# Performance work log

Hardware: AMD Instinct MI355X
Metric: run time of the kernel (lower is better)

## Reference

```python
import jax, jax.numpy as jnp
import numpy as np

N_NODES = 20000
N_REL = 200
DIM = 128
N_EDGES = 200000
N_TIMES = 8


def setup_inputs() -> dict:
    key = jax.random.key(0)
    ks = jax.random.split(key, 12)
    s = 1.0 / np.sqrt(DIM)
    return {
        "edge_index": jax.random.randint(ks[0], (2, N_EDGES), 0, N_NODES),
        "edge_type": jax.random.randint(ks[1], (N_EDGES,), 0, N_REL),
        "edge_time": jax.random.randint(ks[2], (N_EDGES,), 0, N_TIMES),
        "edge_weight": jax.random.uniform(ks[3], (N_EDGES,), dtype=jnp.float32),
        "node_emb": jax.random.normal(ks[4], (N_NODES, DIM), dtype=jnp.float32),
        "rel_emb": jax.random.normal(ks[5], (N_REL, DIM), dtype=jnp.float32),
        "W_enc": jax.random.normal(ks[6], (DIM, DIM), dtype=jnp.float32) * s,
        "Wz": jax.random.normal(ks[7], (DIM, DIM), dtype=jnp.float32) * s,
        "Uz": jax.random.normal(ks[8], (DIM, DIM), dtype=jnp.float32) * s,
        "Wh": jax.random.normal(ks[9], (DIM, DIM), dtype=jnp.float32) * s,
        "Uh": jax.random.normal(ks[10], (DIM, DIM), dtype=jnp.float32) * s,
        "bz": jnp.zeros((DIM,), dtype=jnp.float32),
        "bh": jnp.zeros((DIM,), dtype=jnp.float32),
        "num_times": N_TIMES,
    }


def reference(edge_index, edge_type, edge_time, edge_weight,
              node_emb, rel_emb, W_enc, Wz, Uz, Wh, Uh, bz, bh, num_times):
    # TemporalEncoder.forward: loop over sorted unique timestamps; per-step
    # masked-edge GNN encode (R-GCN lite) then gated SSM cell; state detached.
    src, dst = edge_index[0], edge_index[1]
    rel_e = rel_emb[edge_type]          # [E, D] gather (constant across steps)
    src_e = node_emb[src]               # [E, D]
    n_nodes = node_emb.shape[0]

    def step(state, t):
        m = (edge_time == t).astype(edge_weight.dtype)       # [E]
        msg = src_e * rel_e * (edge_weight * m)[:, None]     # [E, D]
        agg = jax.ops.segment_sum(msg, dst, num_segments=n_nodes)  # [N, D]
        h = jnp.tanh(agg @ W_enc)                            # base_encoder output
        z = jax.nn.sigmoid(h @ Wz + state @ Uz + bz)
        cand = jnp.tanh(h @ Wh + state @ Uh + bh)
        new_state = (1.0 - z) * state + z * cand             # ssm.cell
        return jax.lax.stop_gradient(new_state), new_state   # state.detach()

    state0 = jnp.zeros_like(node_emb)
    _, outs = jax.lax.scan(step, state0, jnp.arange(num_times))
    return outs[-1]  # last_out, shape [N, D]
```

## Files before the change

kernel.cpp:

```cpp
#include <hip/hip_runtime.h>

#define N_NODES 20000
#define N_EDGES 200000
#define DIM 128
#define T_STEPS 8
#define N_TILES (N_NODES / 16)
#define SCAN_N (N_NODES + 1)
#define SCAN_BLKS ((SCAN_N + 1023) / 1024)

typedef short short8 __attribute__((ext_vector_type(8)));
typedef float f32x4 __attribute__((ext_vector_type(4)));

static __device__ __forceinline__ unsigned short f2bf(float f) {
  union { float f; unsigned u; } v; v.f = f;
  unsigned r = v.u + 0x7fffu + ((v.u >> 16) & 1u);
  return (unsigned short)(r >> 16);
}
static __device__ __forceinline__ float fast_tanh(float x) {
  float e = __expf(2.f * x);
  return 1.f - 2.f / (e + 1.f);
}
static __device__ __forceinline__ float fast_sig(float x) {
  return 1.f / (1.f + __expf(-x));
}

__global__ void repack5(const float* __restrict__ w0,
                        const float* __restrict__ w1,
                        const float* __restrict__ w2,
                        const float* __restrict__ w3,
                        const float* __restrict__ w4,
                        unsigned short* __restrict__ pack) {
  int i = blockIdx.x * blockDim.x + threadIdx.x;
  if (i >= 5 * 16384) return;
  int m = i >> 14, r = i & 16383;
  int j = r & 7, lane = (r >> 3) & 63, ks = (r >> 9) & 3, nt = (r >> 11) & 7;
  int n = nt * 16 + (lane & 15);
  int k = ks * 32 + (lane >> 4) * 8 + j;
  const float* w = (m == 0) ? w0 : (m == 1) ? w1 : (m == 2) ? w2
                 : (m == 3) ? w3 : w4;
  pack[i] = f2bf(w[k * DIM + n]);
}

__global__ void hist_k(const int* __restrict__ dst, int* __restrict__ counts) {
  int i = blockIdx.x * blockDim.x + threadIdx.x;
  if (i >= N_EDGES) return;
  atomicAdd(&counts[dst[i]], 1);
}

__global__ void scan1_k(const int* __restrict__ counts,
                        int* __restrict__ base, int* __restrict__ bsum) {
  __shared__ int ls[256];
  int tid = threadIdx.x;
  int i0 = blockIdx.x * 1024 + tid * 4;
  int v[4], ts = 0;
#pragma unroll
  for (int r = 0; r < 4; r++) {
    v[r] = (i0 + r < SCAN_N) ? counts[i0 + r] : 0;
    ts += v[r];
  }
  ls[tid] = ts; __syncthreads();
#pragma unroll
  for (int off = 1; off < 256; off <<= 1) {
    int x = (tid >= off) ? ls[tid - off] : 0;
    __syncthreads(); ls[tid] += x; __syncthreads();
  }
  int run = ls[tid] - ts;
  if (tid == 255) bsum[blockIdx.x] = ls[255];
#pragma unroll
  for (int r = 0; r < 4; r++) {
    if (i0 + r < SCAN_N) base[i0 + r] = run;
    run += v[r];
  }
}

__global__ void scan2_k(int* __restrict__ bsum) {
  __shared__ int ls[256];
  int tid = threadIdx.x;
  int v = (tid < SCAN_BLKS) ? bsum[tid] : 0;
  ls[tid] = v; __syncthreads();
#pragma unroll
  for (int off = 1; off < 256; off <<= 1) {
    int x = (tid >= off) ? ls[tid - off] : 0;
    __syncthreads(); ls[tid] += x; __syncthreads();
  }
  if (tid < SCAN_BLKS) bsum[tid] = ls[tid] - v;
}

__global__ void scan3_k(int* __restrict__ base, const int* __restrict__ bsum) {
  int i = blockIdx.x * blockDim.x + threadIdx.x;
  if (i < SCAN_N) base[i] += bsum[i >> 10];
}

__global__ void fill_k(const int* __restrict__ src, const int* __restrict__ dst,
                       const int* __restrict__ etype, const int* __restrict__ etime,
                       const float* __restrict__ ew,
                       const int* __restrict__ base, int* __restrict__ cursor,
                       unsigned* __restrict__ epack, float* __restrict__ sw) {
  int i = blockIdx.x * blockDim.x + threadIdx.x;
  if (i >= N_EDGES) return;
  int d = dst[i];
  int pos = base[d] + atomicAdd(&cursor[d], 1);
  epack[pos] = (unsigned)src[i] | ((unsigned)etype[i] << 15) | ((unsigned)etime[i] << 23);
  sw[pos] = ew[i];
}

__global__ void gather_k(const int* __restrict__ base,
                         const unsigned* __restrict__ epack,
                         const float* __restrict__ sw,
                         const float* __restrict__ nemb,
                         const float* __restrict__ remb,
                         unsigned short* __restrict__ aggb) {
  int lane = threadIdx.x & 63;
  int node = (blockIdx.x * blockDim.x + threadIdx.x) >> 6;
  int s0 = base[node], s1 = base[node + 1];
  float ax[T_STEPS], ay[T_STEPS];
#pragma unroll
  for (int tt = 0; tt < T_STEPS; tt++) { ax[tt] = 0.f; ay[tt] = 0.f; }
  for (int i = s0; i < s1; i++) {
    unsigned u = epack[i];
    float w = sw[i];
    int s = u & 0x7fff, rt = (u >> 15) & 0xff, t = u >> 23;
    float2 sv = ((const float2*)(nemb + (size_t)s * DIM))[lane];
    float2 rv = ((const float2*)(remb + (size_t)rt * DIM))[lane];
    float m0 = sv.x * rv.x * w;
    float m1 = sv.y * rv.y * w;
#pragma unroll
    for (int tt = 0; tt < T_STEPS; tt++) {
      ax[tt] += (t == tt) ? m0 : 0.f;
      ay[tt] += (t == tt) ? m1 : 0.f;
    }
  }
#pragma unroll
  for (int tt = 0; tt < T_STEPS; tt++) {
    ushort2 o; o.x = f2bf(ax[tt]); o.y = f2bf(ay[tt]);
    ((ushort2*)(aggb + ((size_t)tt * N_NODES + node) * DIM))[lane] = o;
  }
}

__launch_bounds__(512)
__global__ void fused_recur(const unsigned short* __restrict__ aggb,
                            const unsigned short* __restrict__ pack,
                            const float* __restrict__ bz,
                            const float* __restrict__ bh,
                            float* __restrict__ out) {
  __shared__ unsigned short Hb[2][16 * 136];
  __shared__ unsigned short Sb[2][16 * 136];
  int lane = threadIdx.x & 63;
  int nt = threadIdx.x >> 6;
  int tile = blockIdx.x;
  int q = lane >> 4, l15 = lane & 15;
  int row0 = tile * 16;

  short8 wenc[4], wz[4], uz[4], wh[4], uh[4];
#pragma unroll
  for (int ks = 0; ks < 4; ks++) {
    int fo = ((nt * 4 + ks) * 64 + lane) * 8;
    wenc[ks] = *(const short8*)(pack + 16384 * 0 + fo);
    wz[ks]   = *(const short8*)(pack + 16384 * 1 + fo);
    uz[ks]   = *(const short8*)(pack + 16384 * 2 + fo);
    wh[ks]   = *(const short8*)(pack + 16384 * 3 + fo);
    uh[ks]   = *(const short8*)(pack + 16384 * 4 + fo);
  }
  float bzv = bz[nt * 16 + l15];
  float bhv = bh[nt * 16 + l15];

  f32x4 stC = (f32x4){0.f, 0.f, 0.f, 0.f};

  for (int t = 0; t < T_STEPS; t++) {
    f32x4 acch = (f32x4){0.f, 0.f, 0.f, 0.f};
#pragma unroll
    for (int ks = 0; ks < 4; ks++) {
      short8 aA = *(const short8*)(aggb +
          ((size_t)t * N_NODES + row0 + l15) * DIM + ks * 32 + q * 8);
      acch = __builtin_amdgcn_mfma_f32_16x16x32_bf16(aA, wenc[ks], acch, 0, 0, 0);
    }
    unsigned short* hB = Hb[t & 1];
    unsigned short* sB = Sb[t & 1];
#pragma unroll
    for (int r = 0; r < 4; r++) {
      hB[(q * 4 + r) * 136 + nt * 16 + l15] = f2bf(fast_tanh(acch[r]));
      sB[(q * 4 + r) * 136 + nt * 16 + l15] = f2bf(stC[r]);
    }
    __syncthreads();

    short8 hA[4], sA[4];
#pragma unroll
    for (int ks = 0; ks < 4; ks++) {
      hA[ks] = *(const short8*)&hB[l15 * 136 + ks * 32 + q * 8];
      sA[ks] = *(const short8*)&sB[l15 * 136 + ks * 32 + q * 8];
    }

    f32x4 accz = (f32x4){bzv, bzv, bzv, bzv};
    f32x4 accc = (f32x4){bhv, bhv, bhv, bhv};
#pragma unroll
    for (int ks = 0; ks < 4; ks++) {
      accz = __builtin_amdgcn_mfma_f32_16x16x32_bf16(hA[ks], wz[ks], accz, 0, 0, 0);
      accz = __builtin_amdgcn_mfma_f32_16x16x32_bf16(sA[ks], uz[ks], accz, 0, 0, 0);
      accc = __builtin_amdgcn_mfma_f32_16x16x32_bf16(hA[ks], wh[ks], accc, 0, 0, 0);
      accc = __builtin_amdgcn_mfma_f32_16x16x32_bf16(sA[ks], uh[ks], accc, 0, 0, 0);
    }
#pragma unroll
    for (int r = 0; r < 4; r++) {
      float z = fast_sig(accz[r]);
      float c = fast_tanh(accc[r]);
      stC[r] = (1.f - z) * stC[r] + z * c;
    }
  }

#pragma unroll
  for (int r = 0; r < 4; r++)
    out[(size_t)(row0 + q * 4 + r) * DIM + nt * 16 + l15] = stC[r];
}

extern "C" void kernel_launch(void* const* d_in, const int* in_sizes, int n_in,
                              void* d_out, int out_size, void* d_ws, size_t ws_size,
                              hipStream_t stream) {
  const int* eidx  = (const int*)d_in[0];
  const int* src   = eidx;
  const int* dst   = eidx + N_EDGES;
  const int* etype = (const int*)d_in[1];
  const int* etime = (const int*)d_in[2];
  const float* ew   = (const float*)d_in[3];
  const float* nemb = (const float*)d_in[4];
  const float* remb = (const float*)d_in[5];
  const float* Wenc = (const float*)d_in[6];
  const float* Wz   = (const float*)d_in[7];
  const float* Uz   = (const float*)d_in[8];
  const float* Wh   = (const float*)d_in[9];
  const float* Uh   = (const float*)d_in[10];
  const float* bz   = (const float*)d_in[11];
  const float* bh   = (const float*)d_in[12];

  unsigned short* aggb = (unsigned short*)d_ws;
  int* counts = (int*)(aggb + (size_t)T_STEPS * N_NODES * DIM);
  int* cursor = counts + SCAN_N;
  int* bsum   = cursor + N_NODES;
  int* base   = bsum + 64;
  unsigned* epack = (unsigned*)(base + SCAN_N);
  float* sw   = (float*)(epack + N_EDGES);
  unsigned short* pack = (unsigned short*)(sw + N_EDGES);
  float* outp = (float*)d_out;

  hipMemsetAsync(counts, 0, (size_t)(SCAN_N + N_NODES) * sizeof(int), stream);
  repack5<<<(5 * 16384 + 255) / 256, 256, 0, stream>>>(Wenc, Wz, Uz, Wh, Uh, pack);
  hist_k<<<(N_EDGES + 255) / 256, 256, 0, stream>>>(dst, counts);
  scan1_k<<<SCAN_BLKS, 256, 0, stream>>>(counts, base, bsum);
  scan2_k<<<1, 256, 0, stream>>>(bsum);
  scan3_k<<<(SCAN_N + 255) / 256, 256, 0, stream>>>(base, bsum);
  fill_k<<<(N_EDGES + 255) / 256, 256, 0, stream>>>(src, dst, etype, etime, ew,
                                                    base, cursor, epack, sw);
  gather_k<<<N_NODES / 4, 256, 0, stream>>>(base, epack, sw, nemb, remb, aggb);
  fused_recur<<<N_TILES, 512, 0, stream>>>(aggb, pack, bz, bh, outp);
}
```

Before: 223.1 us.

## Split encoder GEMM out of recurrence into separate fully parallel kernel

```diff
diff --git a/kernel.cpp b/kernel.cpp
--- a/kernel.cpp
+++ b/kernel.cpp
@@ -7,6 +7,7 @@
 #define N_TILES (N_NODES / 16)
 #define SCAN_N (N_NODES + 1)
 #define SCAN_BLKS ((SCAN_N + 1023) / 1024)
+#define LSTR 140
 
 typedef short short8 __attribute__((ext_vector_type(8)));
 typedef float f32x4 __attribute__((ext_vector_type(4)));
@@ -137,29 +138,64 @@
   }
 }
 
-__launch_bounds__(512)
-__global__ void fused_recur(const unsigned short* __restrict__ aggb,
-                            const unsigned short* __restrict__ pack,
-                            const float* __restrict__ bz,
-                            const float* __restrict__ bh,
-                            float* __restrict__ out) {
-  __shared__ unsigned short Hb[2][16 * 136];
-  __shared__ unsigned short Sb[2][16 * 136];
+__global__ void enc_H(const unsigned short* __restrict__ aggb,
+                      const unsigned short* __restrict__ pack,
+                      unsigned short* __restrict__ Hbuf) {
+  __shared__ unsigned short hl[4][16 * LSTR];
+  int lane = threadIdx.x & 63;
+  int w = blockIdx.x * 4 + (threadIdx.x >> 6);
+  int t = w & 7, tile = w >> 3;
+  int q = lane >> 4, l15 = lane & 15;
+  int row0 = tile * 16;
+
+  f32x4 acc[8];
+#pragma unroll
+  for (int nt = 0; nt < 8; nt++) acc[nt] = (f32x4){0.f, 0.f, 0.f, 0.f};
+#pragma unroll
+  for (int ks = 0; ks < 4; ks++) {
+    short8 a = *(const short8*)(aggb +
+        ((size_t)t * N_NODES + row0 + l15) * DIM + ks * 32 + q * 8);
+#pragma unroll
+    for (int nt = 0; nt < 8; nt++) {
+      short8 b = *(const short8*)(pack + ((nt * 4 + ks) * 64 + lane) * 8);
+      acc[nt] = __builtin_amdgcn_mfma_f32_16x16x32_bf16(a, b, acc[nt], 0, 0, 0);
+    }
+  }
+  unsigned short* h = hl[threadIdx.x >> 6];
+#pragma unroll
+  for (int nt = 0; nt < 8; nt++)
+#pragma unroll
+    for (int r = 0; r < 4; r++)
+      h[(q * 4 + r) * LSTR + nt * 16 + l15] = f2bf(fast_tanh(acc[nt][r]));
+  __syncthreads();
+#pragma unroll
+  for (int ks = 0; ks < 4; ks++) {
+    short8 v = *(const short8*)&h[l15 * LSTR + ks * 32 + q * 8];
+    *(short8*)(Hbuf + (((size_t)(tile * T_STEPS + t) * 4 + ks) * 64 + lane) * 8) = v;
+  }
+}
+
+__launch_bounds__(512, 4)
+__global__ void recur(const unsigned short* __restrict__ Hbuf,
+                      const unsigned short* __restrict__ pack,
+                      const float* __restrict__ bz,
+                      const float* __restrict__ bh,
+                      float* __restrict__ out) {
+  __shared__ unsigned short Sb[2][16 * LSTR];
   int lane = threadIdx.x & 63;
   int nt = threadIdx.x >> 6;
   int tile = blockIdx.x;
   int q = lane >> 4, l15 = lane & 15;
   int row0 = tile * 16;
 
-  short8 wenc[4], wz[4], uz[4], wh[4], uh[4];
+  short8 wz[4], uz[4], wh[4], uh[4];
 #pragma unroll
   for (int ks = 0; ks < 4; ks++) {
     int fo = ((nt * 4 + ks) * 64 + lane) * 8;
-    wenc[ks] = *(const short8*)(pack + 16384 * 0 + fo);
-    wz[ks]   = *(const short8*)(pack + 16384 * 1 + fo);
-    uz[ks]   = *(const short8*)(pack + 16384 * 2 + fo);
-    wh[ks]   = *(const short8*)(pack + 16384 * 3 + fo);
-    uh[ks]   = *(const short8*)(pack + 16384 * 4 + fo);
+    wz[ks] = *(const short8*)(pack + 16384 * 1 + fo);
+    uz[ks] = *(const short8*)(pack + 16384 * 2 + fo);
+    wh[ks] = *(const short8*)(pack + 16384 * 3 + fo);
+    uh[ks] = *(const short8*)(pack + 16384 * 4 + fo);
   }
   float bzv = bz[nt * 16 + l15];
   float bhv = bh[nt * 16 + l15];
@@ -167,28 +203,23 @@
   f32x4 stC = (f32x4){0.f, 0.f, 0.f, 0.f};
 
   for (int t = 0; t < T_STEPS; t++) {
-    f32x4 acch = (f32x4){0.f, 0.f, 0.f, 0.f};
-#pragma unroll
-    for (int ks = 0; ks < 4; ks++) {
-      short8 aA = *(const short8*)(aggb +
-          ((size_t)t * N_NODES + row0 + l15) * DIM + ks * 32 + q * 8);
-      acch = __builtin_amdgcn_mfma_f32_16x16x32_bf16(aA, wenc[ks], acch, 0, 0, 0);
-    }
-    unsigned short* hB = Hb[t & 1];
     unsigned short* sB = Sb[t & 1];
 #pragma unroll
-    for (int r = 0; r < 4; r++) {
-      hB[(q * 4 + r) * 136 + nt * 16 + l15] = f2bf(fast_tanh(acch[r]));
-      sB[(q * 4 + r) * 136 + nt * 16 + l15] = f2bf(stC[r]);
-    }
+    for (int r = 0; r < 4; r++)
+      sB[(q * 4 + r) * LSTR + nt * 16 + l15] = f2bf(stC[r]);
+
+    short8 hA[4];
+#pragma unroll
+    for (int ks = 0; ks < 4; ks++)
+      hA[ks] = *(const short8*)(Hbuf +
+          (((size_t)(tile * T_STEPS + t) * 4 + ks) * 64 + lane) * 8);
+
     __syncthreads();
 
-    short8 hA[4], sA[4];
-#pragma unroll
-    for (int ks = 0; ks < 4; ks++) {
-      hA[ks] = *(const short8*)&hB[l15 * 136 + ks * 32 + q * 8];
-      sA[ks] = *(const short8*)&sB[l15 * 136 + ks * 32 + q * 8];
-    }
+    short8 sA[4];
+#pragma unroll
+    for (int ks = 0; ks < 4; ks++)
+      sA[ks] = *(const short8*)&sB[l15 * LSTR + ks * 32 + q * 8];
 
     f32x4 accz = (f32x4){bzv, bzv, bzv, bzv};
     f32x4 accc = (f32x4){bhv, bhv, bhv, bhv};
@@ -232,7 +263,8 @@
   const float* bh   = (const float*)d_in[12];
 
   unsigned short* aggb = (unsigned short*)d_ws;
-  int* counts = (int*)(aggb + (size_t)T_STEPS * N_NODES * DIM);
+  unsigned short* Hbuf = aggb + (size_t)T_STEPS * N_NODES * DIM;
+  int* counts = (int*)(Hbuf + (size_t)T_STEPS * N_NODES * DIM);
   int* cursor = counts + SCAN_N;
   int* bsum   = cursor + N_NODES;
   int* base   = bsum + 64;
@@ -250,5 +282,6 @@
   fill_k<<<(N_EDGES + 255) / 256, 256, 0, stream>>>(src, dst, etype, etime, ew,
                                                     base, cursor, epack, sw);
   gather_k<<<N_NODES / 4, 256, 0, stream>>>(base, epack, sw, nemb, remb, aggb);
-  fused_recur<<<N_TILES, 512, 0, stream>>>(aggb, pack, bz, bh, outp);
-}
+  enc_H<<<(N_TILES * T_STEPS) / 4, 256, 0, stream>>>(aggb, pack, Hbuf);
+  recur<<<N_TILES, 512, 0, stream>>>(Hbuf, pack, bz, bh, outp);
+}
```

Result: slower. 235.4 us (+5.5%).

## Process four node tiles per block in recurrent kernel, reloading weights per step

Applied to the files above, without the earlier changes.

```diff
diff --git a/kernel.cpp b/kernel.cpp
--- a/kernel.cpp
+++ b/kernel.cpp
@@ -5,8 +5,10 @@
 #define DIM 128
 #define T_STEPS 8
 #define N_TILES (N_NODES / 16)
+#define TPB 4
 #define SCAN_N (N_NODES + 1)
 #define SCAN_BLKS ((SCAN_N + 1023) / 1024)
+#define LSTR 140
 
 typedef short short8 __attribute__((ext_vector_type(8)));
 typedef float f32x4 __attribute__((ext_vector_type(4)));
@@ -143,73 +145,92 @@
                             const float* __restrict__ bz,
                             const float* __restrict__ bh,
                             float* __restrict__ out) {
-  __shared__ unsigned short Hb[2][16 * 136];
-  __shared__ unsigned short Sb[2][16 * 136];
+  __shared__ unsigned short Hb[2][TPB][16 * LSTR];
+  __shared__ unsigned short Sb[2][TPB][16 * LSTR];
   int lane = threadIdx.x & 63;
   int nt = threadIdx.x >> 6;
-  int tile = blockIdx.x;
   int q = lane >> 4, l15 = lane & 15;
-  int row0 = tile * 16;
-
-  short8 wenc[4], wz[4], uz[4], wh[4], uh[4];
-#pragma unroll
-  for (int ks = 0; ks < 4; ks++) {
-    int fo = ((nt * 4 + ks) * 64 + lane) * 8;
-    wenc[ks] = *(const short8*)(pack + 16384 * 0 + fo);
-    wz[ks]   = *(const short8*)(pack + 16384 * 1 + fo);
-    uz[ks]   = *(const short8*)(pack + 16384 * 2 + fo);
-    wh[ks]   = *(const short8*)(pack + 16384 * 3 + fo);
-    uh[ks]   = *(const short8*)(pack + 16384 * 4 + fo);
-  }
+
+  int tiles[TPB];
+#pragma unroll
+  for (int i = 0; i < TPB; i++) {
+    int tl = blockIdx.x * TPB + i;
+    tiles[i] = (tl < N_TILES) ? tl : (N_TILES - 1);
+  }
+
   float bzv = bz[nt * 16 + l15];
   float bhv = bh[nt * 16 + l15];
 
-  f32x4 stC = (f32x4){0.f, 0.f, 0.f, 0.f};
+  f32x4 stC[TPB];
+#pragma unroll
+  for (int i = 0; i < TPB; i++) stC[i] = (f32x4){0.f, 0.f, 0.f, 0.f};
 
   for (int t = 0; t < T_STEPS; t++) {
-    f32x4 acch = (f32x4){0.f, 0.f, 0.f, 0.f};
+    f32x4 acch[TPB];
+#pragma unroll
+    for (int i = 0; i < TPB; i++) acch[i] = (f32x4){0.f, 0.f, 0.f, 0.f};
 #pragma unroll
     for (int ks = 0; ks < 4; ks++) {
-      short8 aA = *(const short8*)(aggb +
-          ((size_t)t * N_NODES + row0 + l15) * DIM + ks * 32 + q * 8);
-      acch = __builtin_amdgcn_mfma_f32_16x16x32_bf16(aA, wenc[ks], acch, 0, 0, 0);
-    }
-    unsigned short* hB = Hb[t & 1];
-    unsigned short* sB = Sb[t & 1];
-#pragma unroll
-    for (int r = 0; r < 4; r++) {
-      hB[(q * 4 + r) * 136 + nt * 16 + l15] = f2bf(fast_tanh(acch[r]));
-      sB[(q * 4 + r) * 136 + nt * 16 + l15] = f2bf(stC[r]);
+      short8 wenc = *(const short8*)(pack + ((nt * 4 + ks) * 64 + lane) * 8);
+#pragma unroll
+      for (int i = 0; i < TPB; i++) {
+        short8 aA = *(const short8*)(aggb +
+            ((size_t)t * N_NODES + tiles[i] * 16 + l15) * DIM + ks * 32 + q * 8);
+        acch[i] = __builtin_amdgcn_mfma_f32_16x16x32_bf16(aA, wenc, acch[i], 0, 0, 0);
+      }
+    }
+#pragma unroll
+    for (int i = 0; i < TPB; i++) {
+      unsigned short* hB = Hb[t & 1][i];
+      unsigned short* sB = Sb[t & 1][i];
+#pragma unroll
+      for (int r = 0; r < 4; r++) {
+        hB[(q * 4 + r) * LSTR + nt * 16 + l15] = f2bf(fast_tanh(acch[i][r]));
+        sB[(q * 4 + r) * LSTR + nt * 16 + l15] = f2bf(stC[i][r]);
+      }
     }
     __syncthreads();
 
-    short8 hA[4], sA[4];
+    f32x4 accz[TPB], accc[TPB];
+#pragma unroll
+    for (int i = 0; i < TPB; i++) {
+      accz[i] = (f32x4){bzv, bzv, bzv, bzv};
+      accc[i] = (f32x4){bhv, bhv, bhv, bhv};
+    }
 #pragma unroll
     for (int ks = 0; ks < 4; ks++) {
-      hA[ks] = *(const short8*)&hB[l15 * 136 + ks * 32 + q * 8];
-      sA[ks] = *(const short8*)&sB[l15 * 136 + ks * 32 + q * 8];
-    }
-
-    f32x4 accz = (f32x4){bzv, bzv, bzv, bzv};
-    f32x4 accc = (f32x4){bhv, bhv, bhv, bhv};
-#pragma unroll
-    for (int ks = 0; ks < 4; ks++) {
-      accz = __builtin_amdgcn_mfma_f32_16x16x32_bf16(hA[ks], wz[ks], accz, 0, 0, 0);
-      accz = __builtin_amdgcn_mfma_f32_16x16x32_bf16(sA[ks], uz[ks], accz, 0, 0, 0);
-      accc = __builtin_amdgcn_mfma_f32_16x16x32_bf16(hA[ks], wh[ks], accc, 0, 0, 0);
-      accc = __builtin_amdgcn_mfma_f32_16x16x32_bf16(sA[ks], uh[ks], accc, 0, 0, 0);
-    }
-#pragma unroll
-    for (int r = 0; r < 4; r++) {
-      float z = fast_sig(accz[r]);
-      float c = fast_tanh(accc[r]);
-      stC[r] = (1.f - z) * stC[r] + z * c;
-    }
-  }
-
-#pragma unroll
-  for (int r = 0; r < 4; r++)
-    out[(size_t)(row0 + q * 4 + r) * DIM + nt * 16 + l15] = stC[r];
+      int fo = ((nt * 4 + ks) * 64 + lane) * 8;
+      short8 wz = *(const short8*)(pack + 16384 * 1 + fo);
+      short8 uz = *(const short8*)(pack + 16384 * 2 + fo);
+      short8 wh = *(const short8*)(pack + 16384 * 3 + fo);
+      short8 uh = *(const short8*)(pack + 16384 * 4 + fo);
+      int lo = l15 * LSTR + ks * 32 + q * 8;
+#pragma unroll
+      for (int i = 0; i < TPB; i++) {
+        short8 hA = *(const short8*)&Hb[t & 1][i][lo];
+        short8 sA = *(const short8*)&Sb[t & 1][i][lo];
+        accz[i] = __builtin_amdgcn_mfma_f32_16x16x32_bf16(hA, wz, accz[i], 0, 0, 0);
+        accz[i] = __builtin_amdgcn_mfma_f32_16x16x32_bf16(sA, uz, accz[i], 0, 0, 0);
+        accc[i] = __builtin_amdgcn_mfma_f32_16x16x32_bf16(hA, wh, accc[i], 0, 0, 0);
+        accc[i] = __builtin_amdgcn_mfma_f32_16x16x32_bf16(sA, uh, accc[i], 0, 0, 0);
+      }
+    }
+#pragma unroll
+    for (int i = 0; i < TPB; i++) {
+#pragma unroll
+      for (int r = 0; r < 4; r++) {
+        float z = fast_sig(accz[i][r]);
+        float c = fast_tanh(accc[i][r]);
+        stC[i][r] = (1.f - z) * stC[i][r] + z * c;
+      }
+    }
+  }
+
+#pragma unroll
+  for (int i = 0; i < TPB; i++)
+#pragma unroll
+    for (int r = 0; r < 4; r++)
+      out[(size_t)(tiles[i] * 16 + q * 4 + r) * DIM + nt * 16 + l15] = stC[i][r];
 }
 
 extern "C" void kernel_launch(void* const* d_in, const int* in_sizes, int n_in,
@@ -250,5 +271,5 @@
   fill_k<<<(N_EDGES + 255) / 256, 256, 0, stream>>>(src, dst, etype, etime, ew,
                                                     base, cursor, epack, sw);
   gather_k<<<N_NODES / 4, 256, 0, stream>>>(base, epack, sw, nemb, remb, aggb);
-  fused_recur<<<N_TILES, 512, 0, stream>>>(aggb, pack, bz, bh, outp);
-}
+  fused_recur<<<(N_TILES + TPB - 1) / TPB, 512, 0, stream>>>(aggb, pack, bz, bh, outp);
+}
```

Measured after the change: 280.1 us. 1.26x slower.
